# Optimization experiments

Measured on AMD Instinct MI355X. Metric: run time of the kernel, lower is better.

Reference implementation:

```python
import jax, jax.numpy as jnp
import numpy as np


def setup_inputs() -> dict:
    key = jax.random.key(0)
    k1, k2, k3 = jax.random.split(key, 3)
    B, C, H, W = 4, 32, 256, 256
    nw, nh = 16, 16
    K = nw * nh
    pixel_feats = jax.random.normal(k1, (B, C, H, W), dtype=jnp.float32)
    assoc_map = jax.random.uniform(k2, (B, 9, H, W), dtype=jnp.float32)
    index_map = jax.random.randint(k3, (B, H, W), 0, K, dtype=jnp.int32)
    return {
        "pixel_feats": pixel_feats,
        "assoc_map": assoc_map,
        "index_map": index_map,
        "nw_spixels": nw,
        "nh_spixels": nh,
    }


def reference(pixel_feats, assoc_map, index_map, nw_spixels, nh_spixels):
    # pixel_feats: [B,C,H,W], assoc_map: [B,9,H,W] (3x3 superpixel-neighbor
    # association weights, row-major (dy,dx) in {-1,0,1}^2), index_map: [B,H,W]
    # base superpixel id in [0, nw*nh). Output: [B, C, nw*nh].
    B, C, H, W = pixel_feats.shape
    K = nw_spixels * nh_spixels
    P = H * W

    idx = index_map.reshape(B, P).astype(jnp.int32)
    ix = idx % nw_spixels  # base spixel grid x
    iy = idx // nw_spixels  # base spixel grid y

    # 9 relative offsets over the superpixel grid
    dy, dx = jnp.meshgrid(jnp.arange(-1, 2), jnp.arange(-1, 2), indexing="ij")
    dy = dy.reshape(9)
    dx = dx.reshape(9)

    tx = ix[:, None, :] + dx[None, :, None]  # [B,9,P]
    ty = iy[:, None, :] + dy[None, :, None]
    valid = (tx >= 0) & (tx < nw_spixels) & (ty >= 0) & (ty < nh_spixels)
    tgt = jnp.where(valid, ty * nw_spixels + tx, 0)  # [B,9,P]

    w = assoc_map.reshape(B, 9, P) * valid.astype(assoc_map.dtype)  # [B,9,P]

    # fold batch into segment id so a single segment_sum handles all images
    seg = (tgt + jnp.arange(B, dtype=jnp.int32)[:, None, None] * K).reshape(-1)

    wsum = jax.ops.segment_sum(w.reshape(-1), seg, num_segments=B * K)  # [B*K]

    # weighted pixel features scattered into superpixel bins
    contrib = w[:, :, None, :] * pixel_feats.reshape(B, 1, C, P)  # [B,9,C,P]
    contrib = contrib.transpose(0, 1, 3, 2).reshape(-1, C)  # [B*9*P, C]
    fsum = jax.ops.segment_sum(contrib, seg, num_segments=B * K)  # [B*K, C]

    eps = 1e-16
    denom = jnp.where(wsum > eps, wsum, 1.0)
    sp = jnp.where(wsum[:, None] > eps, fsum / denom[:, None], 0.0)
    return sp.reshape(B, K, C).transpose(0, 2, 1)  # [B,C,K]
```

## Files before the change

kernel.cpp:

```cpp
#include <hip/hip_runtime.h>


#define CCH  32
#define KMAX 256
#define FST  (CCH + 1)
#define KFS  (KMAX * FST)

typedef __attribute__((ext_vector_type(4))) int   int4v;
typedef __attribute__((ext_vector_type(4))) float f32x4;

__device__ __forceinline__ unsigned pack_bf16(float a, float b) {
    unsigned ua = __float_as_uint(a);
    unsigned ub = __float_as_uint(b);
    ua = (ua + 0x7FFFu + ((ua >> 16) & 1u)) >> 16;
    ub = (ub + 0x7FFFu + ((ub >> 16) & 1u)) >> 16;
    return ua | (ub << 16);
}
__device__ __forceinline__ unsigned short bf16_1(float a) {
    unsigned ua = __float_as_uint(a);
    return (unsigned short)((ua + 0x7FFFu + ((ua >> 16) & 1u)) >> 16);
}

__device__ __forceinline__ void wg_barrier() {
    asm volatile("s_waitcnt lgkmcnt(0)" ::: "memory");
    __builtin_amdgcn_s_barrier();
}



#define PF_CHUNK(CH, IDXR, WV0, WV1, WV2, FV0, FV1, FV2, FV3)               \
    {                                                                       \
        const int p0n = (blkb * cpb + (CH)) * 64;                           \
        IDXR = ix_b[p0n + pl];                                              \
        WV0 = as_b[(size_t)grp * P + p0n + pl];                             \
        WV1 = as_b[(size_t)(grp + 4) * P + p0n + pl];                       \
        WV2 = (grp == 0) ? as_b[(size_t)8 * P + p0n + pl] : 0.f;            \
        FV0 = *(const float2*)&pf_b[(size_t)(cg     ) * P + p0n + 2 * pp];  \
        FV1 = *(const float2*)&pf_b[(size_t)(cg +  8) * P + p0n + 2 * pp];  \
        FV2 = *(const float2*)&pf_b[(size_t)(cg + 16) * P + p0n + 2 * pp];  \
        FV3 = *(const float2*)&pf_b[(size_t)(cg + 24) * P + p0n + 2 * pp];  \
    }

#define SCATTER_STAGE(IDXR, WV0, WV1, WV2, FV0, FV1, FV2, FV3, O0, O1, O2)  \
    {                                                                       \
        const int iy  = (IDXR) / nw;                                        \
        const int ixx = (IDXR) - iy * nw;                                   \
        const float wvv[3] = {WV0, WV1, WV2};                               \
        int offs[3] = {-1, -1, -1};                                         \
        _Pragma("unroll")                                                   \
        for (int wi = 0; wi < 3; ++wi) {                                    \
            const int j = grp + 4 * wi;                                     \
            if (j >= 9) continue;                                           \
            const int ty = iy + j / 3 - 1;                                  \
            const int tx = ixx + j % 3 - 1;                                 \
            if (tx < 0 || tx >= nw || ty < 0 || ty >= nh) continue;         \
            const int t   = ty * nw + tx;                                   \
            const int off = ((((t >> 4) * 2 + ps_) * 64                     \
                              + (t & 15) + ((q >> 3) << 4)) * 8) + (q & 7); \
            lsA[off] = (short)bf16_1(wvv[wi]);                              \
            offs[wi] = off;                                                 \
        }                                                                   \
        O0 = offs[0]; O1 = offs[1]; O2 = offs[2];                           \
        const float2 fvv[4] = {FV0, FV1, FV2, FV3};                         \
        _Pragma("unroll")                                                   \
        for (int ci = 0; ci < 4; ++ci) {                                    \
            const int c   = cg + 8 * ci;                                    \
            const int off = ((((c >> 4) * 2 + (p2 >> 5)) * 64               \
                              + (c & 15) + ((q2 >> 3) << 4)) * 8) + (q2&7); \
            *(unsigned*)&lsB[off] = pack_bf16(fvv[ci].x, fvv[ci].y);        \
        }                                                                   \
    }

#define MFMA_PHASE()                                                        \
    _Pragma("unroll")                                                       \
    for (int ps = 0; ps < 2; ++ps) {                                        \
        int4v bfr[3];                                                       \
        _Pragma("unroll")                                                   \
        for (int ct = 0; ct < 3; ++ct)                                      \
            bfr[ct] = *(int4v*)&lsB[((ct * 2 + ps) * 64 + lane) * 8];       \
        _Pragma("unroll")                                                   \
        for (int ktl = 0; ktl < 4; ++ktl) {                                 \
            const int kt = wave * 4 + ktl;                                  \
            int4v af = *(int4v*)&lsA[((kt * 2 + ps) * 64 + lane) * 8];      \
            _Pragma("unroll")                                               \
            for (int ct = 0; ct < 3; ++ct) {                                \
                asm("v_mfma_f32_16x16x32_bf16 %0, %1, %2, %0"               \
                    : "+v"(acc[ktl][ct])                                    \
                    : "v"(af), "v"(bfr[ct]));                               \
            }                                                               \
        }                                                                   \
    }

#define UNZERO(O0, O1, O2)                                                  \
    { if ((O0) >= 0) lsA[O0] = 0; if ((O1) >= 0) lsA[O1] = 0;               \
      if ((O2) >= 0) lsA[O2] = 0; }

__global__ __launch_bounds__(256, 4) void spx_mfma_kernel(
    const float* __restrict__ pf,
    const float* __restrict__ assoc,
    const int*   __restrict__ idxmap,
    const int*   __restrict__ nw_p,
    const int*   __restrict__ nh_p,
    float*       __restrict__ part,
    int P, int K, int cpb, int bpbk)
{
    __shared__ __align__(16) short lsA[16 * 2 * 64 * 8];
    __shared__ __align__(16) short lsB[6 * 64 * 8];

    const int tid  = threadIdx.x;
    const int wave = tid >> 6;
    const int lane = tid & 63;
    const int b    = blockIdx.x / bpbk;
    const int blkb = blockIdx.x - b * bpbk;

    const int nw = nw_p[0], nh = nh_p[0];

#pragma unroll
    for (int i = 0; i < 8; ++i)
        *(uint4*)&lsA[(tid + 256 * i) * 8] = make_uint4(0u, 0u, 0u, 0u);
    if (tid < 128) {
        const int reg = 4 + (tid >> 6);
        const int ln  = tid & 63;
        uint4 v = ((ln & 15) == 0)
            ? make_uint4(0x3F803F80u, 0x3F803F80u, 0x3F803F80u, 0x3F803F80u)
            : make_uint4(0u, 0u, 0u, 0u);
        *(uint4*)&lsB[(reg * 64 + ln) * 8] = v;
    }

    const int*   ix_b = idxmap + (size_t)b * P;
    const float* pf_b = pf     + (size_t)b * CCH * P;
    const float* as_b = assoc  + (size_t)b * 9 * P;

    f32x4 acc[4][3];
#pragma unroll
    for (int i = 0; i < 4; ++i)
#pragma unroll
        for (int j = 0; j < 3; ++j) acc[i][j] = f32x4{0.f, 0.f, 0.f, 0.f};

    const int grp = tid >> 6;
    const int pl  = tid & 63;
    const int pp  = tid & 31;
    const int cg  = tid >> 5;
    const int q   = pl & 31;
    const int ps_ = pl >> 5;
    const int p2  = 2 * pp;
    const int q2  = p2 & 31;

    int    idxA, idxB2;
    float  wA0, wA1, wA2, wB0, wB1, wB2;
    float2 fA0, fA1, fA2, fA3, fB0, fB1, fB2, fB3;
    int    oA0, oA1, oA2, oB0, oB1, oB2;

    PF_CHUNK(0, idxA, wA0, wA1, wA2, fA0, fA1, fA2, fA3);
    PF_CHUNK(1, idxB2, wB0, wB1, wB2, fB0, fB1, fB2, fB3);

    wg_barrier();

    for (int ch = 0; ch < cpb; ch += 2) {
        SCATTER_STAGE(idxA, wA0, wA1, wA2, fA0, fA1, fA2, fA3, oA0, oA1, oA2);
        {
            const int chn = (ch + 2 < cpb) ? ch + 2 : cpb - 1;
            PF_CHUNK(chn, idxA, wA0, wA1, wA2, fA0, fA1, fA2, fA3);
        }
        wg_barrier();
        MFMA_PHASE();
        wg_barrier();
        UNZERO(oA0, oA1, oA2);
        wg_barrier();

        SCATTER_STAGE(idxB2, wB0, wB1, wB2, fB0, fB1, fB2, fB3, oB0, oB1, oB2);
        {
            const int chn = (ch + 3 < cpb) ? ch + 3 : cpb - 1;
            PF_CHUNK(chn, idxB2, wB0, wB1, wB2, fB0, fB1, fB2, fB3);
        }
        wg_barrier();
        MFMA_PHASE();
        wg_barrier();
        UNZERO(oB0, oB1, oB2);
        wg_barrier();
    }

    asm volatile("s_nop 7\n\ts_nop 7");

    float* pb = part + (size_t)(b * bpbk + blkb) * KFS;
    const int col = lane & 15;
    const int rw0 = (lane >> 4) * 4;
#pragma unroll
    for (int ktl = 0; ktl < 4; ++ktl) {
        const int kt = wave * 4 + ktl;
#pragma unroll
        for (int ct = 0; ct < 3; ++ct) {
            const int c = ct * 16 + col;
            if (c > CCH) continue;
#pragma unroll
            for (int i = 0; i < 4; ++i) {
                const int k = kt * 16 + rw0 + i;
                pb[(size_t)k * FST + c] = acc[ktl][ct][i];
            }
        }
    }
}

__global__ __launch_bounds__(256) void spx_reduce_div_kernel(
    const float* __restrict__ part,
    float*       __restrict__ out,
    int K, int bpbk)
{
    __shared__ float red[4][4 * FST];

    const int gpb = KMAX / 4;
    const int b   = blockIdx.x / gpb;
    const int g   = blockIdx.x - b * gpb;
    const int w   = threadIdx.x >> 6;
    const int l   = threadIdx.x & 63;

    const float* p = part + (size_t)b * bpbk * KFS + g * (4 * FST);
    const int n = bpbk >> 2;
    float s0 = 0.f, s1 = 0.f, s2 = 0.f;
    for (int m = 0; m < n; m += 2) {
        const float* r0 = p + (size_t)(w + 4 * m) * KFS;
        const float* r1 = p + (size_t)(w + 4 * (m + 1)) * KFS;
        const float a0 = r0[l], a1 = r0[64 + l];
        const float a2 = (l < 4) ? r0[128 + l] : 0.f;
        const float b0 = r1[l], b1 = r1[64 + l];
        const float b2 = (l < 4) ? r1[128 + l] : 0.f;
        s0 += a0 + b0; s1 += a1 + b1; s2 += a2 + b2;
    }
    red[w][l] = s0;
    red[w][64 + l] = s1;
    if (l < 4) red[w][128 + l] = s2;
    __syncthreads();

    if (threadIdx.x < 128) {
        const int c  = threadIdx.x >> 2;
        const int lb = threadIdx.x & 3;
        const float W = red[0][lb * FST + CCH] + red[1][lb * FST + CCH]
                      + red[2][lb * FST + CCH] + red[3][lb * FST + CCH];
        const float v = red[0][lb * FST + c] + red[1][lb * FST + c]
                      + red[2][lb * FST + c] + red[3][lb * FST + c];
        out[((size_t)b * CCH + c) * K + g * 4 + lb] =
            (W > 1e-16f) ? v / W : 0.f;
    }
}

extern "C" void kernel_launch(void* const* d_in, const int* in_sizes, int n_in,
                              void* d_out, int out_size, void* d_ws, size_t ws_size,
                              hipStream_t stream) {
    const float* pf     = (const float*)d_in[0];
    const float* assoc  = (const float*)d_in[1];
    const int*   idxmap = (const int*)d_in[2];
    const int*   nw_p   = (const int*)d_in[3];
    const int*   nh_p   = (const int*)d_in[4];
    float* out = (float*)d_out;

    const int BP = in_sizes[2];
    const int B  = 4;
    const int P  = BP / B;
    const int K  = out_size / (B * CCH);

    int bpbk = 256;
    while ((size_t)B * bpbk * KFS * sizeof(float) > ws_size && bpbk > 64)
        bpbk >>= 1;
    const int cpb = (P / 64) / bpbk;
    float* part = (float*)d_ws;

    spx_mfma_kernel<<<B * bpbk, 256, 0, stream>>>(
        pf, assoc, idxmap, nw_p, nh_p, part, P, K, cpb, bpbk);

    spx_reduce_div_kernel<<<B * (KMAX / 4), 256, 0, stream>>>(
        part, out, K, bpbk);
}
```

Baseline: 107.5 us.

## Double chunk width to 128 pixels, use 512-thread blocks, zero A-tiles inside MFMA loop

Each chunk now covers 128 pixels with 512 threads (8 waves), and each wave owns 2 superpixel tiles instead of 4. The separate scatter-undo pass and one barrier per chunk are removed: each wave clears its A fragments in LDS right after consuming them in the MFMA loop. The grid is halved (bpbk 128), which halves the partial buffers the reduce kernel must sum, at the cost of a larger LDS footprint and possibly lower occupancy per CU.

```diff
diff --git a/kernel.cpp b/kernel.cpp
--- a/kernel.cpp
+++ b/kernel.cpp
@@ -5,6 +5,8 @@
 #define KMAX 256
 #define FST  (CCH + 1)
 #define KFS  (KMAX * FST)
+#define PXC  128
+#define SPS  (PXC / 32)
 
 typedef __attribute__((ext_vector_type(4))) int   int4v;
 typedef __attribute__((ext_vector_type(4))) float f32x4;
@@ -27,10 +29,9 @@
 }
 
 
-
 #define PF_CHUNK(CH, IDXR, WV0, WV1, WV2, FV0, FV1, FV2, FV3)               \
     {                                                                       \
-        const int p0n = (blkb * cpb + (CH)) * 64;                           \
+        const int p0n = (blkb * cpb + (CH)) * PXC;                          \
         IDXR = ix_b[p0n + pl];                                              \
         WV0 = as_b[(size_t)grp * P + p0n + pl];                             \
         WV1 = as_b[(size_t)(grp + 4) * P + p0n + pl];                       \
@@ -41,12 +42,11 @@
         FV3 = *(const float2*)&pf_b[(size_t)(cg + 24) * P + p0n + 2 * pp];  \
     }
 
-#define SCATTER_STAGE(IDXR, WV0, WV1, WV2, FV0, FV1, FV2, FV3, O0, O1, O2)  \
+#define SCATTER_STAGE(IDXR, WV0, WV1, WV2, FV0, FV1, FV2, FV3)              \
     {                                                                       \
         const int iy  = (IDXR) / nw;                                        \
         const int ixx = (IDXR) - iy * nw;                                   \
         const float wvv[3] = {WV0, WV1, WV2};                               \
-        int offs[3] = {-1, -1, -1};                                         \
         _Pragma("unroll")                                                   \
         for (int wi = 0; wi < 3; ++wi) {                                    \
             const int j = grp + 4 * wi;                                     \
@@ -55,47 +55,43 @@
             const int tx = ixx + j % 3 - 1;                                 \
             if (tx < 0 || tx >= nw || ty < 0 || ty >= nh) continue;         \
             const int t   = ty * nw + tx;                                   \
-            const int off = ((((t >> 4) * 2 + ps_) * 64                     \
+            const int off = ((((t >> 4) * SPS + psx) * 64                   \
                               + (t & 15) + ((q >> 3) << 4)) * 8) + (q & 7); \
             lsA[off] = (short)bf16_1(wvv[wi]);                              \
-            offs[wi] = off;                                                 \
         }                                                                   \
-        O0 = offs[0]; O1 = offs[1]; O2 = offs[2];                           \
         const float2 fvv[4] = {FV0, FV1, FV2, FV3};                         \
         _Pragma("unroll")                                                   \
         for (int ci = 0; ci < 4; ++ci) {                                    \
             const int c   = cg + 8 * ci;                                    \
-            const int off = ((((c >> 4) * 2 + (p2 >> 5)) * 64               \
+            const int off = ((((c >> 4) * SPS + (p2 >> 5)) * 64             \
                               + (c & 15) + ((q2 >> 3) << 4)) * 8) + (q2&7); \
             *(unsigned*)&lsB[off] = pack_bf16(fvv[ci].x, fvv[ci].y);        \
         }                                                                   \
     }
 
-#define MFMA_PHASE()                                                        \
+#define MFMA_PHASE_Z()                                                      \
     _Pragma("unroll")                                                       \
-    for (int ps = 0; ps < 2; ++ps) {                                        \
+    for (int ps = 0; ps < SPS; ++ps) {                                      \
         int4v bfr[3];                                                       \
         _Pragma("unroll")                                                   \
         for (int ct = 0; ct < 3; ++ct)                                      \
-            bfr[ct] = *(int4v*)&lsB[((ct * 2 + ps) * 64 + lane) * 8];       \
-        _Pragma("unroll")                                                   \
-        for (int ktl = 0; ktl < 4; ++ktl) {                                 \
-            const int kt = wave * 4 + ktl;                                  \
-            int4v af = *(int4v*)&lsA[((kt * 2 + ps) * 64 + lane) * 8];      \
+            bfr[ct] = *(int4v*)&lsB[((ct * SPS + ps) * 64 + lane) * 8];     \
+        _Pragma("unroll")                                                   \
+        for (int ktl = 0; ktl < 2; ++ktl) {                                 \
+            const int kt  = wave * 2 + ktl;                                 \
+            const int aix = ((kt * SPS + ps) * 64 + lane) * 8;              \
+            int4v af = *(int4v*)&lsA[aix];                                  \
             _Pragma("unroll")                                               \
             for (int ct = 0; ct < 3; ++ct) {                                \
                 asm("v_mfma_f32_16x16x32_bf16 %0, %1, %2, %0"               \
                     : "+v"(acc[ktl][ct])                                    \
                     : "v"(af), "v"(bfr[ct]));                               \
             }                                                               \
+            *(int4v*)&lsA[aix] = (int4v){0, 0, 0, 0};                       \
         }                                                                   \
     }
 
-#define UNZERO(O0, O1, O2)                                                  \
-    { if ((O0) >= 0) lsA[O0] = 0; if ((O1) >= 0) lsA[O1] = 0;               \
-      if ((O2) >= 0) lsA[O2] = 0; }
-
-__global__ __launch_bounds__(256, 4) void spx_mfma_kernel(
+__global__ __launch_bounds__(512, 4) void spx_mfma_kernel(
     const float* __restrict__ pf,
     const float* __restrict__ assoc,
     const int*   __restrict__ idxmap,
@@ -104,8 +100,8 @@
     float*       __restrict__ part,
     int P, int K, int cpb, int bpbk)
 {
-    __shared__ __align__(16) short lsA[16 * 2 * 64 * 8];
-    __shared__ __align__(16) short lsB[6 * 64 * 8];
+    __shared__ __align__(16) short lsA[16 * SPS * 64 * 8];
+    __shared__ __align__(16) short lsB[3 * SPS * 64 * 8];
 
     const int tid  = threadIdx.x;
     const int wave = tid >> 6;
@@ -117,9 +113,9 @@
 
 #pragma unroll
     for (int i = 0; i < 8; ++i)
-        *(uint4*)&lsA[(tid + 256 * i) * 8] = make_uint4(0u, 0u, 0u, 0u);
-    if (tid < 128) {
-        const int reg = 4 + (tid >> 6);
+        *(uint4*)&lsA[(tid + 512 * i) * 8] = make_uint4(0u, 0u, 0u, 0u);
+    if (tid < 256) {
+        const int reg = 2 * SPS + (tid >> 6);
         const int ln  = tid & 63;
         uint4 v = ((ln & 15) == 0)
             ? make_uint4(0x3F803F80u, 0x3F803F80u, 0x3F803F80u, 0x3F803F80u)
@@ -131,25 +127,24 @@
     const float* pf_b = pf     + (size_t)b * CCH * P;
     const float* as_b = assoc  + (size_t)b * 9 * P;
 
-    f32x4 acc[4][3];
-#pragma unroll
-    for (int i = 0; i < 4; ++i)
+    f32x4 acc[2][3];
+#pragma unroll
+    for (int i = 0; i < 2; ++i)
 #pragma unroll
         for (int j = 0; j < 3; ++j) acc[i][j] = f32x4{0.f, 0.f, 0.f, 0.f};
 
-    const int grp = tid >> 6;
-    const int pl  = tid & 63;
-    const int pp  = tid & 31;
-    const int cg  = tid >> 5;
+    const int grp = tid >> 7;
+    const int pl  = tid & 127;
+    const int pp  = tid & 63;
+    const int cg  = tid >> 6;
     const int q   = pl & 31;
-    const int ps_ = pl >> 5;
+    const int psx = pl >> 5;
     const int p2  = 2 * pp;
     const int q2  = p2 & 31;
 
     int    idxA, idxB2;
     float  wA0, wA1, wA2, wB0, wB1, wB2;
     float2 fA0, fA1, fA2, fA3, fB0, fB1, fB2, fB3;
-    int    oA0, oA1, oA2, oB0, oB1, oB2;
 
     PF_CHUNK(0, idxA, wA0, wA1, wA2, fA0, fA1, fA2, fA3);
     PF_CHUNK(1, idxB2, wB0, wB1, wB2, fB0, fB1, fB2, fB3);
@@ -157,26 +152,22 @@
     wg_barrier();
 
     for (int ch = 0; ch < cpb; ch += 2) {
-        SCATTER_STAGE(idxA, wA0, wA1, wA2, fA0, fA1, fA2, fA3, oA0, oA1, oA2);
+        SCATTER_STAGE(idxA, wA0, wA1, wA2, fA0, fA1, fA2, fA3);
         {
             const int chn = (ch + 2 < cpb) ? ch + 2 : cpb - 1;
             PF_CHUNK(chn, idxA, wA0, wA1, wA2, fA0, fA1, fA2, fA3);
         }
         wg_barrier();
-        MFMA_PHASE();
-        wg_barrier();
-        UNZERO(oA0, oA1, oA2);
-        wg_barrier();
-
-        SCATTER_STAGE(idxB2, wB0, wB1, wB2, fB0, fB1, fB2, fB3, oB0, oB1, oB2);
+        MFMA_PHASE_Z();
+        wg_barrier();
+
+        SCATTER_STAGE(idxB2, wB0, wB1, wB2, fB0, fB1, fB2, fB3);
         {
             const int chn = (ch + 3 < cpb) ? ch + 3 : cpb - 1;
             PF_CHUNK(chn, idxB2, wB0, wB1, wB2, fB0, fB1, fB2, fB3);
         }
         wg_barrier();
-        MFMA_PHASE();
-        wg_barrier();
-        UNZERO(oB0, oB1, oB2);
+        MFMA_PHASE_Z();
         wg_barrier();
     }
 
@@ -186,8 +177,8 @@
     const int col = lane & 15;
     const int rw0 = (lane >> 4) * 4;
 #pragma unroll
-    for (int ktl = 0; ktl < 4; ++ktl) {
-        const int kt = wave * 4 + ktl;
+    for (int ktl = 0; ktl < 2; ++ktl) {
+        const int kt = wave * 2 + ktl;
 #pragma unroll
         for (int ct = 0; ct < 3; ++ct) {
             const int c = ct * 16 + col;
@@ -258,13 +249,13 @@
     const int P  = BP / B;
     const int K  = out_size / (B * CCH);
 
-    int bpbk = 256;
-    while ((size_t)B * bpbk * KFS * sizeof(float) > ws_size && bpbk > 64)
+    int bpbk = 128;
+    while ((size_t)B * bpbk * KFS * sizeof(float) > ws_size && bpbk > 32)
         bpbk >>= 1;
-    const int cpb = (P / 64) / bpbk;
+    const int cpb = (P / PXC) / bpbk;
     float* part = (float*)d_ws;
 
-    spx_mfma_kernel<<<B * bpbk, 256, 0, stream>>>(
+    spx_mfma_kernel<<<B * bpbk, 512, 0, stream>>>(
         pf, assoc, idxmap, nw_p, nh_p, part, P, K, cpb, bpbk);
 
     spx_reduce_div_kernel<<<B * (KMAX / 4), 256, 0, stream>>>(
```

Measured after the change: 103.8 us. -3.5%, faster.
